# Kernel optimization log

Measured on AMD Instinct MI355X. Metric: run time of the kernel, lower is better.

Reference implementation:

```python
import math
import jax, jax.numpy as jnp
import numpy as np

B, Q, M = 4, 512, 8192
LOC_D, SENS_D, EMB_D = 8, 256, 512


def setup_inputs() -> dict:
    key = jax.random.key(0)
    ks = jax.random.split(key, 6)
    location = jax.random.normal(ks[0], (B, Q, LOC_D), dtype=jnp.float32)
    # sds must be positive (they are squared and logged); keep them away from 0
    location_sd = jax.random.uniform(ks[1], (B, Q, LOC_D), dtype=jnp.float32) * 0.9 + 0.1
    memory_locations = jax.random.normal(ks[2], (B, M, LOC_D), dtype=jnp.float32)
    memory_location_sds = jax.random.uniform(ks[3], (B, M, LOC_D), dtype=jnp.float32) * 0.9 + 0.1
    memory_senses = jax.random.normal(ks[4], (B, M, EMB_D), dtype=jnp.float32)
    # sensory_read_proj: Linear(embed_dim -> sensory_dim, bias=False)
    W_read = jax.random.normal(ks[5], (SENS_D, EMB_D), dtype=jnp.float32) / math.sqrt(EMB_D)
    return {
        "location": location,
        "location_sd": location_sd,
        "memory_locations": memory_locations,
        "memory_location_sds": memory_location_sds,
        "memory_senses": memory_senses,
        "W_read": W_read,
    }


def reference(location, location_sd, memory_locations, memory_location_sds, memory_senses, W_read):
    # BidirectionalMemory.read with match_threshold=None, detach_* True (stop_gradient)
    mem_loc = jax.lax.stop_gradient(memory_locations)
    mem_sd = jax.lax.stop_gradient(memory_location_sds)
    mem_sense = jax.lax.stop_gradient(memory_senses)

    # (B,Q,1,D) - (B,1,M,D) -> (B,Q,M,D)
    delta = location[:, :, None, :] - mem_loc[:, None, :, :]
    var = location_sd[:, :, None, :] ** 2 + mem_sd[:, None, :, :] ** 2
    d = delta.shape[-1]
    # -0.5 * sum((delta^2 / (var+eps))^2) - 0.5*log(2pi)*D - sum(log(var))
    log_aff = (
        -0.5 * jnp.sum((delta ** 2 / (var + 1e-8)) ** 2, axis=-1)
        - 0.5 * math.log(2.0 * math.pi) * d
        - jnp.sum(jnp.log(var), axis=-1)
    )  # (B,Q,M)
    weights = jax.nn.softmax(log_aff, axis=-1)  # (B,Q,M)
    pre_sense = jnp.einsum("bqm,bme->bqe", weights, mem_sense)  # (B,Q,EMB_D)
    sense = jnp.einsum("bqe,se->bqs", pre_sense, W_read)  # (B,Q,SENS_D)
    return sense
```

## Files before the change

### kernel.cpp

```cpp
#include <hip/hip_runtime.h>
#include <hip/hip_bf16.h>

#define BB 4
#define QQ 512
#define MM 8192
#define DD 8
#define EE 512
#define SS 256

#define QG 16
#define MSP 8
#define MSL (MM / MSP)
#define NQG (BB * QQ / QG)

using f32x4  = __attribute__((ext_vector_type(4))) float;
using bf16x8 = __attribute__((ext_vector_type(8))) short;

static __device__ __forceinline__ unsigned short f2bf(float f) {
  union { __hip_bfloat16 h; unsigned short u; } v;
  v.h = __float2bfloat16(f);
  return v.u;
}

__global__ __launch_bounds__(256) void k_proj(
    const float* __restrict__ V, const float* __restrict__ W,
    unsigned short* __restrict__ projT)
{
  const int m0 = blockIdx.x * 128;
  const int s0 = blockIdx.y * 128;
  const int b  = blockIdx.z;
  const int t = threadIdx.x, lane = t & 63, wv = t >> 6;
  const int wr = wv >> 1, wc = wv & 1;

  __shared__ short lA[128 * 64];
  __shared__ short lB[128 * 64];

  f32x4 acc[4][4] = {};

  const float* Wp = W + (size_t)s0 * EE;
  const float* Vp = V + (size_t)b * MM * EE + (size_t)m0 * EE;

  const int r0 = t >> 4;
  const int c0 = (t & 15) * 4;
  const int swz = (r0 & 7) << 3;

  float4 ra[8], rb[8];

#define P_LOADS(K0)                                                        \
  _Pragma("unroll")                                                        \
  for (int j = 0; j < 8; ++j) {                                            \
    const int row = j * 16 + r0;                                           \
    ra[j] = *reinterpret_cast<const float4*>(&Wp[(size_t)row * EE + (K0) + c0]); \
    rb[j] = *reinterpret_cast<const float4*>(&Vp[(size_t)row * EE + (K0) + c0]); \
  }

  P_LOADS(0)

  for (int ki = 0; ki < 8; ++ki) {
    __syncthreads();
#pragma unroll
    for (int j = 0; j < 8; ++j) {
      const int row = j * 16 + r0;
      const int idx = (row * 64 + c0) ^ swz;
      ushort4 da, db;
      da.x = f2bf(ra[j].x); da.y = f2bf(ra[j].y); da.z = f2bf(ra[j].z); da.w = f2bf(ra[j].w);
      db.x = f2bf(rb[j].x); db.y = f2bf(rb[j].y); db.z = f2bf(rb[j].z); db.w = f2bf(rb[j].w);
      *reinterpret_cast<ushort4*>(&lA[idx]) = da;
      *reinterpret_cast<ushort4*>(&lB[idx]) = db;
    }
    if (ki < 7) { P_LOADS((ki + 1) * 64) }
    __syncthreads();

#pragma unroll
    for (int kk = 0; kk < 2; ++kk) {
      const int kofs = kk * 32 + (lane >> 4) * 8;
      const int r15 = lane & 15;
      bf16x8 af[4], bfv[4];
#pragma unroll
      for (int mi = 0; mi < 4; ++mi) {
        int row = wr * 64 + mi * 16 + r15;
        af[mi] = *reinterpret_cast<const bf16x8*>(&lA[(row * 64 + kofs) ^ ((row & 7) << 3)]);
      }
#pragma unroll
      for (int ni = 0; ni < 4; ++ni) {
        int row = wc * 64 + ni * 16 + r15;
        bfv[ni] = *reinterpret_cast<const bf16x8*>(&lB[(row * 64 + kofs) ^ ((row & 7) << 3)]);
      }
#pragma unroll
      for (int mi = 0; mi < 4; ++mi)
#pragma unroll
        for (int ni = 0; ni < 4; ++ni)
          acc[mi][ni] = __builtin_amdgcn_mfma_f32_16x16x32_bf16(af[mi], bfv[ni], acc[mi][ni], 0, 0, 0);
    }
  }
#undef P_LOADS

  unsigned short* outp = projT + (size_t)b * SS * MM;
  const int fr = (lane >> 4) * 4;
  const int fc = lane & 15;
#pragma unroll
  for (int mi = 0; mi < 4; ++mi)
#pragma unroll
    for (int ni = 0; ni < 4; ++ni)
#pragma unroll
      for (int r = 0; r < 4; ++r) {
        int s = s0 + wr * 64 + mi * 16 + fr + r;
        int m = m0 + wc * 64 + ni * 16 + fc;
        outp[(size_t)s * MM + m] = f2bf(acc[mi][ni][r]);
      }
}

__global__ __launch_bounds__(256, 2) void k_fused(
    const float* __restrict__ loc, const float* __restrict__ locsd,
    const float* __restrict__ mloc, const float* __restrict__ msd,
    const unsigned short* __restrict__ projT,
    float* __restrict__ opart, float* __restrict__ mn_g,
    float* __restrict__ sum_g)
{
  __shared__ float la_s[8 * MSL];
  __shared__ unsigned short p_s[QG * MSL];
  __shared__ float lx_s[QG][DD], ls2_s[QG][DD];
  __shared__ float red[QG][4];

  const int hw = blockIdx.x;
  const int ms = hw & 7;
  const int qg = hw >> 3;
  const int b  = qg >> 5;
  const int q0 = (qg & 31) * QG;
  const int t = threadIdx.x, lane = t & 63, wv = t >> 6;

  if (t < QG * DD) {
    const int qq = t >> 3, d = t & 7;
    const int base = (b * QQ + q0 + qq) * DD + d;
    lx_s[qq][d] = loc[base];
    float s = locsd[base];
    ls2_s[qq][d] = __builtin_fmaf(s, s, 1e-8f);
  }

  const float4* ml4 = reinterpret_cast<const float4*>(mloc + (size_t)b * MM * DD);
  const float4* ms4 = reinterpret_cast<const float4*>(msd  + (size_t)b * MM * DD);
  float mlv[2][2][DD], ms2[2][2][DD];
#pragma unroll
  for (int c = 0; c < 2; ++c)
#pragma unroll
    for (int p = 0; p < 2; ++p) {
      const int m = ms * MSL + c * 512 + 2 * t + p;
      float4 a0 = ml4[2 * m], a1 = ml4[2 * m + 1];
      float4 s0 = ms4[2 * m], s1 = ms4[2 * m + 1];
      mlv[c][p][0] = a0.x; mlv[c][p][1] = a0.y; mlv[c][p][2] = a0.z; mlv[c][p][3] = a0.w;
      mlv[c][p][4] = a1.x; mlv[c][p][5] = a1.y; mlv[c][p][6] = a1.z; mlv[c][p][7] = a1.w;
      ms2[c][p][0] = s0.x * s0.x; ms2[c][p][1] = s0.y * s0.y;
      ms2[c][p][2] = s0.z * s0.z; ms2[c][p][3] = s0.w * s0.w;
      ms2[c][p][4] = s1.x * s1.x; ms2[c][p][5] = s1.y * s1.y;
      ms2[c][p][6] = s1.z * s1.z; ms2[c][p][7] = s1.w * s1.w;
    }
  __syncthreads();

  float rs[QG];
#pragma unroll
  for (int q = 0; q < QG; ++q) rs[q] = 0.f;

#pragma unroll
  for (int sub = 0; sub < 2; ++sub) {
    float mn8[8];
#pragma unroll
    for (int q8 = 0; q8 < 8; ++q8) {
      const int q = sub * 8 + q8;
      float lxq[DD], lsq[DD];
#pragma unroll
      for (int d = 0; d < DD; d += 4) {
        float4 v1 = *reinterpret_cast<const float4*>(&lx_s[q][d]);
        lxq[d] = v1.x; lxq[d + 1] = v1.y; lxq[d + 2] = v1.z; lxq[d + 3] = v1.w;
        float4 v2 = *reinterpret_cast<const float4*>(&ls2_s[q][d]);
        lsq[d] = v2.x; lsq[d + 1] = v2.y; lsq[d + 2] = v2.z; lsq[d + 3] = v2.w;
      }
      float mnq = 3.4e38f;
#pragma unroll
      for (int c = 0; c < 2; ++c) {
        float la2[2];
#pragma unroll
        for (int p = 0; p < 2; ++p) {
          float ssum = 0.f, pr = 1.f;
#pragma unroll
          for (int d = 0; d < DD; ++d) {
            float v  = lsq[d] + ms2[c][p][d];
            float r  = __builtin_amdgcn_rcpf(v);
            float dl = lxq[d] - mlv[c][p][d];
            float d2 = dl * dl;
            float tt = d2 * r;
            ssum = __builtin_fmaf(tt, tt, ssum);
            pr *= v;
          }
          la2[p] = __builtin_fmaf(ssum, 0.72134752f, __builtin_amdgcn_logf(pr));
          mnq = fminf(mnq, la2[p]);
        }
        float2 wr2; wr2.x = la2[0]; wr2.y = la2[1];
        *reinterpret_cast<float2*>(&la_s[q8 * MSL + c * 512 + 2 * t]) = wr2;
      }
      mn8[q8] = mnq;
    }
#pragma unroll
    for (int q8 = 0; q8 < 8; ++q8) {
      float v = mn8[q8];
#pragma unroll
      for (int off = 32; off; off >>= 1) v = fminf(v, __shfl_xor(v, off, 64));
      if (lane == 0) red[q8][wv] = v;
    }
    __syncthreads();
    float mnb[8];
#pragma unroll
    for (int q8 = 0; q8 < 8; ++q8) {
      mnb[q8] = fminf(fminf(red[q8][0], red[q8][1]), fminf(red[q8][2], red[q8][3]));
      if (t == q8)
        mn_g[((size_t)qg * MSP + ms) * QG + sub * 8 + q8] = mnb[q8];
    }
    __syncthreads();
#pragma unroll
    for (int q8 = 0; q8 < 8; ++q8) {
      const int q = sub * 8 + q8;
      const int swz = (q & 7) << 4;
#pragma unroll
      for (int c = 0; c < 2; ++c) {
        float2 la2 = *reinterpret_cast<const float2*>(&la_s[q8 * MSL + c * 512 + 2 * t]);
        float e0 = __builtin_amdgcn_exp2f(mnb[q8] - la2.x);
        float e1 = __builtin_amdgcn_exp2f(mnb[q8] - la2.y);
        rs[q] += e0 + e1;
        unsigned int pk = (unsigned int)f2bf(e0) | ((unsigned int)f2bf(e1) << 16);
        *reinterpret_cast<unsigned int*>(
            (char*)p_s + (((q * MSL + c * 512 + 2 * t) * 2) ^ swz)) = pk;
      }
    }
  }

  __syncthreads();
#pragma unroll
  for (int q = 0; q < QG; ++q) {
    float v = rs[q];
#pragma unroll
    for (int off = 32; off; off >>= 1) v += __shfl_xor(v, off, 64);
    if (lane == 0) red[q][wv] = v;
  }
  __syncthreads();
#pragma unroll
  for (int q = 0; q < QG; ++q)
    if (t == q)
      sum_g[((size_t)qg * MSP + ms) * QG + q] = red[q][0] + red[q][1] + red[q][2] + red[q][3];

  const unsigned short* pTb = projT + (size_t)b * SS * MM + (size_t)ms * MSL;
  const int s0w = wv * 64;
  const int qf = lane & 15;
  const int kf = (lane >> 4) * 8;
  const int aswz = (qf & 7) << 4;
  f32x4 acc[4] = {};

#define LDA(CH) (*reinterpret_cast<const bf16x8*>( \
    (const char*)p_s + (((qf * MSL + (CH) * 32 + kf) * 2) ^ aswz)))
#define LOADB(U, CH)                                                        \
  _Pragma("unroll")                                                         \
  for (int ni = 0; ni < 4; ++ni)                                            \
    U[ni] = *reinterpret_cast<const uint4*>(                                \
        pTb + (size_t)(s0w + ni * 16 + qf) * MM + (CH) * 32 + kf);

  uint4 u0[4], u1[4];
  bf16x8 a0, a1;
  LOADB(u0, 0) a0 = LDA(0);
#pragma unroll 2
  for (int ch = 0; ch < 32; ch += 2) {
    LOADB(u1, ch + 1) a1 = LDA(ch + 1);
#pragma unroll
    for (int ni = 0; ni < 4; ++ni)
      acc[ni] = __builtin_amdgcn_mfma_f32_16x16x32_bf16(
          a0, *reinterpret_cast<const bf16x8*>(&u0[ni]), acc[ni], 0, 0, 0);
    if (ch + 2 < 32) { LOADB(u0, ch + 2) a0 = LDA(ch + 2); }
#pragma unroll
    for (int ni = 0; ni < 4; ++ni)
      acc[ni] = __builtin_amdgcn_mfma_f32_16x16x32_bf16(
          a1, *reinterpret_cast<const bf16x8*>(&u1[ni]), acc[ni], 0, 0, 0);
  }
#undef LDA
#undef LOADB

  float* op = opart + ((size_t)qg * MSP + ms) * (QG * SS);
#pragma unroll
  for (int ni = 0; ni < 4; ++ni)
#pragma unroll
    for (int r = 0; r < 4; ++r) {
      const int q = (lane >> 4) * 4 + r;
      const int s = s0w + ni * 16 + qf;
      op[q * SS + s] = acc[ni][r];
    }
}

__global__ __launch_bounds__(256) void k_merge(
    const float* __restrict__ opart, const float* __restrict__ mn_g,
    const float* __restrict__ sum_g, float* __restrict__ out)
{
  const int row = blockIdx.x * 4 + (threadIdx.x >> 6);
  const int lane = threadIdx.x & 63;
  const int qg = row >> 4, q = row & 15;

  const float* mnp = mn_g  + (size_t)qg * MSP * QG + q;
  const float* smp = sum_g + (size_t)qg * MSP * QG + q;
  float mns[MSP], gmn = 3.4e38f;
#pragma unroll
  for (int i = 0; i < MSP; ++i) { mns[i] = mnp[i * QG]; gmn = fminf(gmn, mns[i]); }
  float gsum = 0.f, sc[MSP];
#pragma unroll
  for (int i = 0; i < MSP; ++i) {
    sc[i] = __builtin_amdgcn_exp2f(gmn - mns[i]);
    gsum = __builtin_fmaf(smp[i * QG], sc[i], gsum);
  }
  float o[4] = {0.f, 0.f, 0.f, 0.f};
  const float* ob = opart + (size_t)qg * MSP * (QG * SS) + q * SS;
#pragma unroll
  for (int i = 0; i < MSP; ++i)
#pragma unroll
    for (int j = 0; j < 4; ++j)
      o[j] = __builtin_fmaf(ob[(size_t)i * (QG * SS) + j * 64 + lane], sc[i], o[j]);
  const float inv = 1.0f / gsum;
  float* orow = out + (size_t)row * SS;
#pragma unroll
  for (int j = 0; j < 4; ++j) orow[j * 64 + lane] = o[j] * inv;
}


extern "C" void kernel_launch(void* const* d_in, const int* in_sizes, int n_in,
                              void* d_out, int out_size, void* d_ws, size_t ws_size,
                              hipStream_t stream) {
  const float* loc    = (const float*)d_in[0];
  const float* locsd  = (const float*)d_in[1];
  const float* mloc   = (const float*)d_in[2];
  const float* msd    = (const float*)d_in[3];
  const float* msense = (const float*)d_in[4];
  const float* wread  = (const float*)d_in[5];
  float* out = (float*)d_out;

  const size_t proj_bytes  = (size_t)BB * SS * MM * 2;
  const size_t opart_bytes = (size_t)NQG * MSP * QG * SS * 4;
  const size_t mn_bytes    = (size_t)NQG * MSP * QG * 4;
  if (ws_size < proj_bytes + opart_bytes + 2 * mn_bytes) return;

  unsigned short* projT = (unsigned short*)d_ws;
  float* opart = (float*)((char*)d_ws + proj_bytes);
  float* mn_g  = (float*)((char*)d_ws + proj_bytes + opart_bytes);
  float* sum_g = (float*)((char*)d_ws + proj_bytes + opart_bytes + mn_bytes);

  hipLaunchKernelGGL(k_proj, dim3(MM / 128, SS / 128, BB), dim3(256), 0, stream,
                     msense, wread, projT);
  hipLaunchKernelGGL(k_fused, dim3(NQG * MSP), dim3(256), 0, stream,
                     loc, locsd, mloc, msd, projT, opart, mn_g, sum_g);
  hipLaunchKernelGGL(k_merge, dim3(BB * QQ / 4), dim3(256), 0, stream,
                     opart, mn_g, sum_g, out);
}
```

Baseline: 115.6 us.

## Double fused-kernel block size to 512 threads and keep log-affinities in registers

The fused affinity/softmax/MFMA kernel now launches 512 threads per block, so each thread handles two memory slots instead of four and each wave covers 32 output columns instead of 64. The la_s shared buffer is removed: log-affinities stay in registers, and the per-query min and sum reductions happen inline per query through 8-wave shared arrays. This cuts shared memory use and per-thread registers to allow more resident waves, and drops one barrier per half-pass. In exchange there are more shuffle reductions, and each wave loads fewer B tiles per A fragment, which lowers data reuse in the MFMA phase.

```diff
diff --git a/kernel.cpp b/kernel.cpp
--- a/kernel.cpp
+++ b/kernel.cpp
@@ -110,17 +110,17 @@
       }
 }
 
-__global__ __launch_bounds__(256, 2) void k_fused(
+__global__ __launch_bounds__(512, 4) void k_fused(
     const float* __restrict__ loc, const float* __restrict__ locsd,
     const float* __restrict__ mloc, const float* __restrict__ msd,
     const unsigned short* __restrict__ projT,
     float* __restrict__ opart, float* __restrict__ mn_g,
     float* __restrict__ sum_g)
 {
-  __shared__ float la_s[8 * MSL];
   __shared__ unsigned short p_s[QG * MSL];
   __shared__ float lx_s[QG][DD], ls2_s[QG][DD];
-  __shared__ float red[QG][4];
+  __shared__ float redmin[QG][8];
+  __shared__ float redsum[QG][8];
 
   const int hw = blockIdx.x;
   const int ms = hw & 7;
@@ -139,30 +139,26 @@
 
   const float4* ml4 = reinterpret_cast<const float4*>(mloc + (size_t)b * MM * DD);
   const float4* ms4 = reinterpret_cast<const float4*>(msd  + (size_t)b * MM * DD);
-  float mlv[2][2][DD], ms2[2][2][DD];
-#pragma unroll
-  for (int c = 0; c < 2; ++c)
-#pragma unroll
-    for (int p = 0; p < 2; ++p) {
-      const int m = ms * MSL + c * 512 + 2 * t + p;
-      float4 a0 = ml4[2 * m], a1 = ml4[2 * m + 1];
-      float4 s0 = ms4[2 * m], s1 = ms4[2 * m + 1];
-      mlv[c][p][0] = a0.x; mlv[c][p][1] = a0.y; mlv[c][p][2] = a0.z; mlv[c][p][3] = a0.w;
-      mlv[c][p][4] = a1.x; mlv[c][p][5] = a1.y; mlv[c][p][6] = a1.z; mlv[c][p][7] = a1.w;
-      ms2[c][p][0] = s0.x * s0.x; ms2[c][p][1] = s0.y * s0.y;
-      ms2[c][p][2] = s0.z * s0.z; ms2[c][p][3] = s0.w * s0.w;
-      ms2[c][p][4] = s1.x * s1.x; ms2[c][p][5] = s1.y * s1.y;
-      ms2[c][p][6] = s1.z * s1.z; ms2[c][p][7] = s1.w * s1.w;
-    }
+  float mlv[2][DD], ms2[2][DD];
+#pragma unroll
+  for (int p = 0; p < 2; ++p) {
+    const int m = ms * MSL + 2 * t + p;
+    float4 a0 = ml4[2 * m], a1 = ml4[2 * m + 1];
+    float4 s0 = ms4[2 * m], s1 = ms4[2 * m + 1];
+    mlv[p][0] = a0.x; mlv[p][1] = a0.y; mlv[p][2] = a0.z; mlv[p][3] = a0.w;
+    mlv[p][4] = a1.x; mlv[p][5] = a1.y; mlv[p][6] = a1.z; mlv[p][7] = a1.w;
+    ms2[p][0] = s0.x * s0.x; ms2[p][1] = s0.y * s0.y;
+    ms2[p][2] = s0.z * s0.z; ms2[p][3] = s0.w * s0.w;
+    ms2[p][4] = s1.x * s1.x; ms2[p][5] = s1.y * s1.y;
+    ms2[p][6] = s1.z * s1.z; ms2[p][7] = s1.w * s1.w;
+  }
   __syncthreads();
 
-  float rs[QG];
-#pragma unroll
-  for (int q = 0; q < QG; ++q) rs[q] = 0.f;
+  const size_t g_base = ((size_t)qg * MSP + ms) * QG;
 
 #pragma unroll
   for (int sub = 0; sub < 2; ++sub) {
-    float mn8[8];
+    float la_r[8][2];
 #pragma unroll
     for (int q8 = 0; q8 < 8; ++q8) {
       const int q = sub * 8 + q8;
@@ -176,113 +172,97 @@
       }
       float mnq = 3.4e38f;
 #pragma unroll
-      for (int c = 0; c < 2; ++c) {
-        float la2[2];
-#pragma unroll
-        for (int p = 0; p < 2; ++p) {
-          float ssum = 0.f, pr = 1.f;
-#pragma unroll
-          for (int d = 0; d < DD; ++d) {
-            float v  = lsq[d] + ms2[c][p][d];
-            float r  = __builtin_amdgcn_rcpf(v);
-            float dl = lxq[d] - mlv[c][p][d];
-            float d2 = dl * dl;
-            float tt = d2 * r;
-            ssum = __builtin_fmaf(tt, tt, ssum);
-            pr *= v;
-          }
-          la2[p] = __builtin_fmaf(ssum, 0.72134752f, __builtin_amdgcn_logf(pr));
-          mnq = fminf(mnq, la2[p]);
+      for (int p = 0; p < 2; ++p) {
+        float ssum = 0.f, pr = 1.f;
+#pragma unroll
+        for (int d = 0; d < DD; ++d) {
+          float v  = lsq[d] + ms2[p][d];
+          float r  = __builtin_amdgcn_rcpf(v);
+          float dl = lxq[d] - mlv[p][d];
+          float d2 = dl * dl;
+          float tt = d2 * r;
+          ssum = __builtin_fmaf(tt, tt, ssum);
+          pr *= v;
         }
-        float2 wr2; wr2.x = la2[0]; wr2.y = la2[1];
-        *reinterpret_cast<float2*>(&la_s[q8 * MSL + c * 512 + 2 * t]) = wr2;
-      }
-      mn8[q8] = mnq;
-    }
-#pragma unroll
-    for (int q8 = 0; q8 < 8; ++q8) {
-      float v = mn8[q8];
-#pragma unroll
-      for (int off = 32; off; off >>= 1) v = fminf(v, __shfl_xor(v, off, 64));
-      if (lane == 0) red[q8][wv] = v;
+        la_r[q8][p] = __builtin_fmaf(ssum, 0.72134752f, __builtin_amdgcn_logf(pr));
+        mnq = fminf(mnq, la_r[q8][p]);
+      }
+#pragma unroll
+      for (int off = 32; off; off >>= 1) mnq = fminf(mnq, __shfl_xor(mnq, off, 64));
+      if (lane == 0) redmin[q][wv] = mnq;
     }
     __syncthreads();
     float mnb[8];
 #pragma unroll
     for (int q8 = 0; q8 < 8; ++q8) {
-      mnb[q8] = fminf(fminf(red[q8][0], red[q8][1]), fminf(red[q8][2], red[q8][3]));
-      if (t == q8)
-        mn_g[((size_t)qg * MSP + ms) * QG + sub * 8 + q8] = mnb[q8];
-    }
-    __syncthreads();
+      const int q = sub * 8 + q8;
+      float m2 = redmin[q][0];
+#pragma unroll
+      for (int w = 1; w < 8; ++w) m2 = fminf(m2, redmin[q][w]);
+      mnb[q8] = m2;
+      if (t == q8) mn_g[g_base + q] = m2;
+    }
 #pragma unroll
     for (int q8 = 0; q8 < 8; ++q8) {
       const int q = sub * 8 + q8;
       const int swz = (q & 7) << 4;
-#pragma unroll
-      for (int c = 0; c < 2; ++c) {
-        float2 la2 = *reinterpret_cast<const float2*>(&la_s[q8 * MSL + c * 512 + 2 * t]);
-        float e0 = __builtin_amdgcn_exp2f(mnb[q8] - la2.x);
-        float e1 = __builtin_amdgcn_exp2f(mnb[q8] - la2.y);
-        rs[q] += e0 + e1;
-        unsigned int pk = (unsigned int)f2bf(e0) | ((unsigned int)f2bf(e1) << 16);
-        *reinterpret_cast<unsigned int*>(
-            (char*)p_s + (((q * MSL + c * 512 + 2 * t) * 2) ^ swz)) = pk;
-      }
+      float e0 = __builtin_amdgcn_exp2f(mnb[q8] - la_r[q8][0]);
+      float e1 = __builtin_amdgcn_exp2f(mnb[q8] - la_r[q8][1]);
+      unsigned int pk = (unsigned int)f2bf(e0) | ((unsigned int)f2bf(e1) << 16);
+      *reinterpret_cast<unsigned int*>(
+          (char*)p_s + (((q * MSL + 2 * t) * 2) ^ swz)) = pk;
+      float v = e0 + e1;
+#pragma unroll
+      for (int off = 32; off; off >>= 1) v += __shfl_xor(v, off, 64);
+      if (lane == 0) redsum[q][wv] = v;
     }
   }
 
   __syncthreads();
-#pragma unroll
-  for (int q = 0; q < QG; ++q) {
-    float v = rs[q];
-#pragma unroll
-    for (int off = 32; off; off >>= 1) v += __shfl_xor(v, off, 64);
-    if (lane == 0) red[q][wv] = v;
-  }
-  __syncthreads();
-#pragma unroll
-  for (int q = 0; q < QG; ++q)
-    if (t == q)
-      sum_g[((size_t)qg * MSP + ms) * QG + q] = red[q][0] + red[q][1] + red[q][2] + red[q][3];
+  if (t < QG) {
+    float s = 0.f;
+#pragma unroll
+    for (int w = 0; w < 8; ++w) s += redsum[t][w];
+    sum_g[g_base + t] = s;
+  }
 
   const unsigned short* pTb = projT + (size_t)b * SS * MM + (size_t)ms * MSL;
-  const int s0w = wv * 64;
+  const int s0w = wv * 32;
   const int qf = lane & 15;
   const int kf = (lane >> 4) * 8;
   const int aswz = (qf & 7) << 4;
-  f32x4 acc[4] = {};
+  f32x4 acc[2] = {};
 
 #define LDA(CH) (*reinterpret_cast<const bf16x8*>( \
     (const char*)p_s + (((qf * MSL + (CH) * 32 + kf) * 2) ^ aswz)))
 #define LOADB(U, CH)                                                        \
   _Pragma("unroll")                                                         \
-  for (int ni = 0; ni < 4; ++ni)                                            \
+  for (int ni = 0; ni < 2; ++ni)                                            \
     U[ni] = *reinterpret_cast<const uint4*>(                                \
         pTb + (size_t)(s0w + ni * 16 + qf) * MM + (CH) * 32 + kf);
 
-  uint4 u0[4], u1[4];
+  uint4 u0[2], u1[2];
   bf16x8 a0, a1;
   LOADB(u0, 0) a0 = LDA(0);
 #pragma unroll 2
   for (int ch = 0; ch < 32; ch += 2) {
     LOADB(u1, ch + 1) a1 = LDA(ch + 1);
 #pragma unroll
-    for (int ni = 0; ni < 4; ++ni)
+    for (int ni = 0; ni < 2; ++ni)
       acc[ni] = __builtin_amdgcn_mfma_f32_16x16x32_bf16(
           a0, *reinterpret_cast<const bf16x8*>(&u0[ni]), acc[ni], 0, 0, 0);
     if (ch + 2 < 32) { LOADB(u0, ch + 2) a0 = LDA(ch + 2); }
 #pragma unroll
-    for (int ni = 0; ni < 4; ++ni)
+    for (int ni = 0; ni < 2; ++ni)
       acc[ni] = __builtin_amdgcn_mfma_f32_16x16x32_bf16(
           a1, *reinterpret_cast<const bf16x8*>(&u1[ni]), acc[ni], 0, 0, 0);
   }
 #undef LDA
 #undef LOADB
 
-  float* op = opart + ((size_t)qg * MSP + ms) * (QG * SS);
-#pragma unroll
-  for (int ni = 0; ni < 4; ++ni)
+  float* op = opart + g_base * SS;
+#pragma unroll
+  for (int ni = 0; ni < 2; ++ni)
 #pragma unroll
     for (int r = 0; r < 4; ++r) {
       const int q = (lane >> 4) * 4 + r;
@@ -347,7 +327,7 @@
 
   hipLaunchKernelGGL(k_proj, dim3(MM / 128, SS / 128, BB), dim3(256), 0, stream,
                      msense, wread, projT);
-  hipLaunchKernelGGL(k_fused, dim3(NQG * MSP), dim3(256), 0, stream,
+  hipLaunchKernelGGL(k_fused, dim3(NQG * MSP), dim3(512), 0, stream,
                      loc, locsd, mloc, msd, projT, opart, mn_g, sum_g);
   hipLaunchKernelGGL(k_merge, dim3(BB * QQ / 4), dim3(256), 0, stream,
                      opart, mn_g, sum_g, out);
```

After: 111.1 us. 1.04x faster.
